# Kernel optimization log

Hardware: AMD Instinct MI355X
Metric: run time of the kernel (lower is better)

## Reference

```python
import jax, jax.numpy as jnp
import numpy as np

B, T, D, H = 4, 2048, 1024, 16
HD = D // H  # head_dim = 64

def setup_inputs() -> dict:
    key = jax.random.key(0)
    ks = jax.random.split(key, 5)
    s = 0.02
    return {
        "x": jax.random.normal(ks[0], (B, T, D), jnp.float32),
        "Wq": jax.random.normal(ks[1], (D, D), jnp.float32) * s,
        "Wk": jax.random.normal(ks[2], (D, D), jnp.float32) * s,
        "Wv": jax.random.normal(ks[3], (D, D), jnp.float32) * s,
        "Wo": jax.random.normal(ks[4], (D, D), jnp.float32) * s,
        "bo": jnp.zeros((D,), jnp.float32),
    }

def reference(x, Wq, Wk, Wv, Wo, bo):
    b, t, _ = x.shape
    # projections (no qkv bias), split into heads: [b, H, t, hd]
    def split_heads(y):
        return y.reshape(b, t, H, HD).transpose(0, 2, 1, 3)
    q = split_heads(x @ Wq)
    k = split_heads(x @ Wk)
    v = split_heads(x @ Wv)
    # causal attention scores, scaled by sqrt(head_dim)
    scores = jnp.einsum('bhqd,bhkd->bhqk', q, k) / jnp.sqrt(jnp.float32(HD))
    causal = jnp.tril(jnp.ones((t, t), bool))  # True = keep
    scores = jnp.where(causal, scores, -jnp.inf)
    w = jax.nn.softmax(scores, axis=-1)
    # dropout p=0.0 -> identity (eval-mode math)
    z = jnp.einsum('bhqk,bhkd->bhqd', w, v)
    z = z.transpose(0, 2, 1, 3).reshape(b, t, D)
    return z @ Wo + bo
```

## Files before the change

### kernel.cpp

```cpp
#include <hip/hip_runtime.h>
#include <hip/hip_bf16.h>

#define B_ 4
#define T_ 2048
#define D_ 1024
#define H_ 16
#define HD_ 64
#define M_ (B_*T_)

#define QSCALE (0.125f * 1.44269504088896f)

typedef __bf16  bf16x8 __attribute__((ext_vector_type(8)));
typedef __bf16  bf16x4 __attribute__((ext_vector_type(4)));
typedef float   f32x4  __attribute__((ext_vector_type(4)));
typedef ushort  u16x8  __attribute__((ext_vector_type(8)));

__device__ __forceinline__ ushort f2bf(float f) {
  union { float f; uint u; } c; c.f = f;
  uint u = c.u;
  uint r = (u + 0x7FFFu + ((u >> 16) & 1u)) >> 16;
  return (ushort)r;
}

__device__ __forceinline__ void gload_lds16(const void* g, void* l) {
  __builtin_amdgcn_global_load_lds(
      (const __attribute__((address_space(1))) void*)g,
      (__attribute__((address_space(3))) void*)l, 16, 0, 0);
}

__global__ __launch_bounds__(256) void cast_bf16(const float* __restrict__ x,
                                                 ushort* __restrict__ o, int n) {
  int i = (blockIdx.x * 256 + threadIdx.x) * 8;
  if (i >= n) return;
  float4 a = *(const float4*)&x[i];
  float4 b = *(const float4*)&x[i + 4];
  u16x8 r;
  r[0] = f2bf(a.x); r[1] = f2bf(a.y); r[2] = f2bf(a.z); r[3] = f2bf(a.w);
  r[4] = f2bf(b.x); r[5] = f2bf(b.y); r[6] = f2bf(b.z); r[7] = f2bf(b.w);
  *(u16x8*)&o[i] = r;
}

__global__ __launch_bounds__(256) void transw(const float* __restrict__ W0,
                                              const float* __restrict__ W1,
                                              const float* __restrict__ W2,
                                              const float* __restrict__ W3,
                                              ushort* __restrict__ Wt) {
  __shared__ float tile[32][33];
  const float* W = (blockIdx.z == 0) ? W0 : (blockIdx.z == 1) ? W1
                  : (blockIdx.z == 2) ? W2 : W3;
  ushort* dst = Wt + (size_t)blockIdx.z * D_ * D_;
  int tx = threadIdx.x & 31, ty = threadIdx.x >> 5;
  int bx = blockIdx.x, by = blockIdx.y;
  #pragma unroll
  for (int i = 0; i < 4; ++i)
    tile[ty + i * 8][tx] = W[(by * 32 + ty + i * 8) * D_ + bx * 32 + tx];
  __syncthreads();
  #pragma unroll
  for (int i = 0; i < 4; ++i)
    dst[(bx * 32 + ty + i * 8) * D_ + by * 32 + tx] = f2bf(tile[tx][ty + i * 8]);
}

template<int EPI>
__global__ __launch_bounds__(256, 2) void gemm_bt(const ushort* __restrict__ A,
                                                  const ushort* __restrict__ Bt,
                                                  const float* __restrict__ bias,
                                                  ushort* __restrict__ Qb,
                                                  ushort* __restrict__ Kb,
                                                  ushort* __restrict__ Vt,
                                                  float* __restrict__ Out) {
  constexpr int MI  = (EPI == 0) ? 8 : 4;
  constexpr int BM  = MI * 32;
  constexpr int MSP = MI * 16;
  __shared__ __align__(16) ushort As[BM * 64];
  __shared__ __align__(16) ushort Bs[128 * 64];
  const int tid = threadIdx.x;
  const int l   = tid & 63;
  const int wid = tid >> 6;
  const int lr  = l & 15, lg = l >> 4;
  const int wm  = wid >> 1, wn = wid & 1;

  const int nwgx = gridDim.x;
  int bid = blockIdx.y * nwgx + blockIdx.x;
  int cpx = (nwgx * gridDim.y) >> 3;
  int swz = (bid & 7) * cpx + (bid >> 3);
  const int m0 = (swz / nwgx) * BM;
  const int n0 = (swz % nwgx) * 128;

  const int srow = l >> 3;
  const int sce  = ((l & 7) ^ srow) * 8;
  const int xr   = (lr & 7) << 4;
  const int ce0  = ((0  + lg * 16) ^ xr) >> 1;
  const int ce1  = ((64 + lg * 16) ^ xr) >> 1;

  f32x4 acc[MI][4];
  #pragma unroll
  for (int mi = 0; mi < MI; ++mi)
    #pragma unroll
    for (int ni = 0; ni < 4; ++ni)
      acc[mi][ni] = (f32x4){0.f, 0.f, 0.f, 0.f};

  #pragma unroll 1
  for (int k0 = 0; k0 < 1024; k0 += 64) {
    #pragma unroll
    for (int j = 0; j < MI; ++j) {
      int c = wid * MI + j;
      gload_lds16(&A[(size_t)(m0 + c * 8 + srow) * 1024 + k0 + sce],
                  &As[c * 512]);
    }
    #pragma unroll
    for (int j = 0; j < 4; ++j) {
      int c = wid * 4 + j;
      gload_lds16(&Bt[(size_t)(n0 + c * 8 + srow) * 1024 + k0 + sce],
                  &Bs[c * 512]);
    }
    __syncthreads();
    #pragma unroll
    for (int kk = 0; kk < 2; ++kk) {
      const int ce = kk ? ce1 : ce0;
      bf16x8 af[MI], bfv[4];
      #pragma unroll
      for (int mi = 0; mi < MI; ++mi)
        af[mi] = *(const bf16x8*)&As[(wm * MSP + mi * 16 + lr) * 64 + ce];
      #pragma unroll
      for (int ni = 0; ni < 4; ++ni)
        bfv[ni] = *(const bf16x8*)&Bs[(wn * 64 + ni * 16 + lr) * 64 + ce];
      __builtin_amdgcn_s_setprio(1);
      #pragma unroll
      for (int mi = 0; mi < MI; ++mi)
        #pragma unroll
        for (int ni = 0; ni < 4; ++ni)
          acc[mi][ni] = __builtin_amdgcn_mfma_f32_16x16x32_bf16(
              af[mi], bfv[ni], acc[mi][ni], 0, 0, 0);
      __builtin_amdgcn_s_setprio(0);
    }
    __syncthreads();
  }

  if (EPI == 0) {
    const int g = n0 >> 10;
    const int h = ((n0 & 1023) >> 6) + wn;
    if (g == 2) {
      #pragma unroll
      for (int mi = 0; mi < MI; ++mi) {
        int rr0 = m0 + wm * MSP + mi * 16 + lg * 4;
        int b = rr0 >> 11, t = rr0 & 2047;
        #pragma unroll
        for (int ni = 0; ni < 4; ++ni) {
          int hd = ni * 16 + lr;
          bf16x4 p4;
          #pragma unroll
          for (int r = 0; r < 4; ++r) p4[r] = (__bf16)acc[mi][ni][r];
          *(bf16x4*)&Vt[((size_t)(b * H_ + h) * HD_ + hd) * T_ + t] = p4;
        }
      }
    } else {
      #pragma unroll
      for (int mi = 0; mi < MI; ++mi)
        #pragma unroll
        for (int r = 0; r < 4; ++r) {
          int rr = m0 + wm * MSP + mi * 16 + lg * 4 + r;
          int b = rr >> 11, t = rr & 2047;
          #pragma unroll
          for (int ni = 0; ni < 4; ++ni) {
            int hd = ni * 16 + lr;
            float v = acc[mi][ni][r];
            if (g == 0) Qb[((size_t)(b * H_ + h) * T_ + t) * HD_ + hd] = f2bf(v * QSCALE);
            else        Kb[((size_t)(b * H_ + h) * T_ + t) * HD_ + hd] = f2bf(v);
          }
        }
    }
  } else {
    #pragma unroll
    for (int mi = 0; mi < MI; ++mi)
      #pragma unroll
      for (int ni = 0; ni < 4; ++ni) {
        int col = n0 + wn * 64 + ni * 16 + lr;
        float bv = bias[col];
        #pragma unroll
        for (int r = 0; r < 4; ++r) {
          int rr = m0 + wm * MSP + mi * 16 + lg * 4 + r;
          Out[(size_t)rr * 1024 + col] = acc[mi][ni][r] + bv;
        }
      }
  }
}

__global__ __launch_bounds__(256, 3) void attn_fwd(const ushort* __restrict__ Qb,
                                                   const ushort* __restrict__ Kb,
                                                   const ushort* __restrict__ Vt,
                                                   ushort* __restrict__ Z) {
  __shared__ __align__(16) ushort Ks[2][64 * 64];
  __shared__ __align__(16) ushort Vs[2][64 * 64];
  __shared__ __align__(16) ushort Plds[4][32 * 72];
  const int tid = threadIdx.x;
  const int l   = tid & 63;
  const int wid = tid >> 6;
  const int lr  = l & 15, lg = l >> 4;
  const int s   = blockIdx.x;
  const int idx = s >> 3;
  const int bh  = (s & 7) + 8 * (idx & 7);
  const int j   = 15 - (idx >> 3);
  const int q0  = j * 128;
  const int qw  = q0 + wid * 32;
  const int NT  = 2 * j + 2;
  const int myDiag = 2 * j + (wid >> 1);
  const ushort* Qh = Qb + (size_t)bh * T_ * HD_;
  const ushort* Kh = Kb + (size_t)bh * T_ * HD_;
  const ushort* Vh = Vt + (size_t)bh * HD_ * T_;
  ushort* Pl = &Plds[wid][0];

  const int srow = l >> 3;
  const int sce  = ((l & 7) ^ srow) * 8;
  const int xrE  = (lr & 7) * 8;
  const int ceK0 = (lg * 8) ^ xrE;
  const int ceK1 = (32 + lg * 8) ^ xrE;

  const int foff = lr * 64 + lg * 8;
  bf16x8 bq[2][2];
  #pragma unroll
  for (int qi = 0; qi < 2; ++qi)
    #pragma unroll
    for (int kk = 0; kk < 2; ++kk)
      bq[qi][kk] = *(const bf16x8*)&Qh[(qw + qi * 16) * 64 + kk * 32 + foff];

  f32x4 o[2][4];
  float l_[2] = {0.f, 0.f};
  #pragma unroll
  for (int mi = 0; mi < 2; ++mi)
    #pragma unroll
    for (int hi = 0; hi < 4; ++hi)
      o[mi][hi] = (f32x4){0.f, 0.f, 0.f, 0.f};

#define STAGEKV(BUF, KT)                                                        \
  {                                                                             \
    _Pragma("unroll")                                                           \
    for (int c = 0; c < 2; ++c) {                                               \
      int i = wid * 2 + c;                                                      \
      gload_lds16(&Kh[(size_t)((KT) * 64 + i * 8 + srow) * 64 + sce],           \
                  &Ks[BUF][i * 512]);                                           \
      gload_lds16(&Vh[(size_t)(i * 8 + srow) * T_ + (KT) * 64 + sce],           \
                  &Vs[BUF][i * 512]);                                           \
    }                                                                           \
  }

  STAGEKV(0, 0);
  __syncthreads();

  #pragma unroll 1
  for (int kt = 0; kt < NT; ++kt) {
    const int cur = kt & 1;
    if (kt + 1 < NT) STAGEKV(cur ^ 1, kt + 1);

    if (kt <= myDiag) {
      bf16x8 bk[4][2];
      #pragma unroll
      for (int ki = 0; ki < 4; ++ki) {
        bk[ki][0] = *(const bf16x8*)&Ks[cur][(ki * 16 + lr) * 64 + ceK0];
        bk[ki][1] = *(const bf16x8*)&Ks[cur][(ki * 16 + lr) * 64 + ceK1];
      }
      f32x4 st[4][2];
      #pragma unroll
      for (int ki = 0; ki < 4; ++ki)
        #pragma unroll
        for (int qi = 0; qi < 2; ++qi)
          st[ki][qi] = (f32x4){0.f, 0.f, 0.f, 0.f};
      __builtin_amdgcn_s_setprio(1);
      #pragma unroll
      for (int kk = 0; kk < 2; ++kk)
        #pragma unroll
        for (int ki = 0; ki < 4; ++ki)
          #pragma unroll
          for (int qi = 0; qi < 2; ++qi)
            st[ki][qi] = __builtin_amdgcn_mfma_f32_16x16x32_bf16(
                bk[ki][kk], bq[qi][kk], st[ki][qi], 0, 0, 0);
      __builtin_amdgcn_s_setprio(0);

      if (kt == myDiag) {
        const int qbase = qw - kt * 64;
        #pragma unroll
        for (int qi = 0; qi < 2; ++qi) {
          int qoff = qbase + qi * 16 + lr;
          #pragma unroll
          for (int ki = 0; ki < 4; ++ki)
            #pragma unroll
            for (int r = 0; r < 4; ++r)
              if (ki * 16 + lg * 4 + r > qoff) st[ki][qi][r] = -1e30f;
        }
      }

      #pragma unroll
      for (int qi = 0; qi < 2; ++qi) {
        float rs = 0.f;
        #pragma unroll
        for (int ki = 0; ki < 4; ++ki) {
          bf16x4 p4;
          #pragma unroll
          for (int r = 0; r < 4; ++r) {
            float p = exp2f(st[ki][qi][r]);
            rs += p;
            p4[r] = (__bf16)p;
          }
          *(bf16x4*)&Pl[(qi * 16 + lr) * 72 + ki * 16 + lg * 4] = p4;
        }
        l_[qi] += rs;
      }

      bf16x8 bv[4][2];
      #pragma unroll
      for (int hi = 0; hi < 4; ++hi) {
        bv[hi][0] = *(const bf16x8*)&Vs[cur][(hi * 16 + lr) * 64 + ceK0];
        bv[hi][1] = *(const bf16x8*)&Vs[cur][(hi * 16 + lr) * 64 + ceK1];
      }
      bf16x8 ap[2][2];
      #pragma unroll
      for (int mi = 0; mi < 2; ++mi)
        #pragma unroll
        for (int kk = 0; kk < 2; ++kk)
          ap[mi][kk] = *(const bf16x8*)&Pl[(mi * 16 + lr) * 72 + kk * 32 + lg * 8];
      __builtin_amdgcn_s_setprio(1);
      #pragma unroll
      for (int kk = 0; kk < 2; ++kk)
        #pragma unroll
        for (int mi = 0; mi < 2; ++mi)
          #pragma unroll
          for (int hi = 0; hi < 4; ++hi)
            o[mi][hi] = __builtin_amdgcn_mfma_f32_16x16x32_bf16(
                ap[mi][kk], bv[hi][kk], o[mi][hi], 0, 0, 0);
      __builtin_amdgcn_s_setprio(0);
    }
    __syncthreads();
  }
#undef STAGEKV

  #pragma unroll
  for (int mi = 0; mi < 2; ++mi) {
    l_[mi] += __shfl_xor(l_[mi], 16);
    l_[mi] += __shfl_xor(l_[mi], 32);
  }
  const int b = bh >> 4, h = bh & 15;
  #pragma unroll
  for (int mi = 0; mi < 2; ++mi)
    #pragma unroll
    for (int r = 0; r < 4; ++r) {
      float lv = __shfl(l_[mi], lg * 4 + r);
      float rinv = 1.f / lv;
      int t = qw + mi * 16 + lg * 4 + r;
      #pragma unroll
      for (int hi = 0; hi < 4; ++hi)
        Z[((size_t)(b * T_ + t)) * D_ + h * 64 + hi * 16 + lr] =
            f2bf(o[mi][hi][r] * rinv);
    }
}

extern "C" void kernel_launch(void* const* d_in, const int* in_sizes, int n_in,
                              void* d_out, int out_size, void* d_ws, size_t ws_size,
                              hipStream_t stream) {
  const float* x  = (const float*)d_in[0];
  const float* Wq = (const float*)d_in[1];
  const float* Wk = (const float*)d_in[2];
  const float* Wv = (const float*)d_in[3];
  const float* Wo = (const float*)d_in[4];
  const float* bo = (const float*)d_in[5];
  float* out = (float*)d_out;

  char* ws = (char*)d_ws;
  ushort* xb = (ushort*)(ws);
  ushort* Wt = (ushort*)(ws + 16777216);
  ushort* Qb = (ushort*)(ws + 25165824);
  ushort* Kb = (ushort*)(ws + 41943040);
  ushort* Vt = (ushort*)(ws + 58720256);
  ushort* Zb = (ushort*)(ws + 75497472);

  cast_bf16<<<4096, 256, 0, stream>>>(x, xb, M_ * D_);
  transw<<<dim3(32, 32, 4), 256, 0, stream>>>(Wq, Wk, Wv, Wo, Wt);
  gemm_bt<0><<<dim3(24, 32), 256, 0, stream>>>(xb, Wt, nullptr, Qb, Kb, Vt, nullptr);
  attn_fwd<<<1024, 256, 0, stream>>>(Qb, Kb, Vt, Zb);
  gemm_bt<1><<<dim3(8, 64), 256, 0, stream>>>(Zb, Wt + 3 * 1024 * 1024, bo,
                                              nullptr, nullptr, nullptr, out);
}
```

Baseline: 164.2 us.

## Swap MFMA operands for vectorized GEMM epilogues and compute softmax row sums via MFMA

In the projection GEMM, Q/K and output-projection tiles now swap MFMA A/B operands, so each lane holds four consecutive columns. This lets the epilogue write bf16x4 and float4 stores instead of scattered scalar stores. In attention, the row sum of P is computed by an extra MFMA against a ones vector rather than by scalar adds and cross-lane shuffles, and it is already laid out per row for normalization. The cost is extra MFMA work per tile and an operand-order branch in the GEMM inner loop.

```diff
diff --git a/kernel.cpp b/kernel.cpp
--- a/kernel.cpp
+++ b/kernel.cpp
@@ -86,6 +86,9 @@
   const int m0 = (swz / nwgx) * BM;
   const int n0 = (swz % nwgx) * 128;
 
+  const int g = (EPI == 0) ? (n0 >> 10) : -1;
+  const bool swp = (EPI == 1) || (g != 2);
+
   const int srow = l >> 3;
   const int sce  = ((l & 7) ^ srow) * 8;
   const int xr   = (lr & 7) << 4;
@@ -125,20 +128,28 @@
       for (int ni = 0; ni < 4; ++ni)
         bfv[ni] = *(const bf16x8*)&Bs[(wn * 64 + ni * 16 + lr) * 64 + ce];
       __builtin_amdgcn_s_setprio(1);
-      #pragma unroll
-      for (int mi = 0; mi < MI; ++mi)
-        #pragma unroll
-        for (int ni = 0; ni < 4; ++ni)
-          acc[mi][ni] = __builtin_amdgcn_mfma_f32_16x16x32_bf16(
-              af[mi], bfv[ni], acc[mi][ni], 0, 0, 0);
+      if (swp) {
+        #pragma unroll
+        for (int mi = 0; mi < MI; ++mi)
+          #pragma unroll
+          for (int ni = 0; ni < 4; ++ni)
+            acc[mi][ni] = __builtin_amdgcn_mfma_f32_16x16x32_bf16(
+                bfv[ni], af[mi], acc[mi][ni], 0, 0, 0);
+      } else {
+        #pragma unroll
+        for (int mi = 0; mi < MI; ++mi)
+          #pragma unroll
+          for (int ni = 0; ni < 4; ++ni)
+            acc[mi][ni] = __builtin_amdgcn_mfma_f32_16x16x32_bf16(
+                af[mi], bfv[ni], acc[mi][ni], 0, 0, 0);
+      }
       __builtin_amdgcn_s_setprio(0);
     }
     __syncthreads();
   }
 
   if (EPI == 0) {
-    const int g = n0 >> 10;
-    const int h = ((n0 & 1023) >> 6) + wn;
+    const int hb = ((n0 & 1023) >> 6) + wn;
     if (g == 2) {
       #pragma unroll
       for (int mi = 0; mi < MI; ++mi) {
@@ -150,38 +161,42 @@
           bf16x4 p4;
           #pragma unroll
           for (int r = 0; r < 4; ++r) p4[r] = (__bf16)acc[mi][ni][r];
-          *(bf16x4*)&Vt[((size_t)(b * H_ + h) * HD_ + hd) * T_ + t] = p4;
+          *(bf16x4*)&Vt[((size_t)(b * H_ + hb) * HD_ + hd) * T_ + t] = p4;
         }
       }
     } else {
-      #pragma unroll
-      for (int mi = 0; mi < MI; ++mi)
-        #pragma unroll
-        for (int r = 0; r < 4; ++r) {
-          int rr = m0 + wm * MSP + mi * 16 + lg * 4 + r;
-          int b = rr >> 11, t = rr & 2047;
-          #pragma unroll
-          for (int ni = 0; ni < 4; ++ni) {
-            int hd = ni * 16 + lr;
-            float v = acc[mi][ni][r];
-            if (g == 0) Qb[((size_t)(b * H_ + h) * T_ + t) * HD_ + hd] = f2bf(v * QSCALE);
-            else        Kb[((size_t)(b * H_ + h) * T_ + t) * HD_ + hd] = f2bf(v);
-          }
-        }
+      const float sc = (g == 0) ? QSCALE : 1.0f;
+      ushort* dst = (g == 0) ? Qb : Kb;
+      #pragma unroll
+      for (int mi = 0; mi < MI; ++mi) {
+        int rr = m0 + wm * MSP + mi * 16 + lr;
+        int b = rr >> 11, t = rr & 2047;
+        #pragma unroll
+        for (int ni = 0; ni < 4; ++ni) {
+          int hd0 = ni * 16 + lg * 4;
+          bf16x4 p4;
+          #pragma unroll
+          for (int r = 0; r < 4; ++r) p4[r] = (__bf16)(acc[mi][ni][r] * sc);
+          *(bf16x4*)&dst[((size_t)(b * H_ + hb) * T_ + t) * HD_ + hd0] = p4;
+        }
+      }
     }
   } else {
     #pragma unroll
-    for (int mi = 0; mi < MI; ++mi)
+    for (int mi = 0; mi < MI; ++mi) {
+      int rr = m0 + wm * MSP + mi * 16 + lr;
       #pragma unroll
       for (int ni = 0; ni < 4; ++ni) {
-        int col = n0 + wn * 64 + ni * 16 + lr;
-        float bv = bias[col];
-        #pragma unroll
-        for (int r = 0; r < 4; ++r) {
-          int rr = m0 + wm * MSP + mi * 16 + lg * 4 + r;
-          Out[(size_t)rr * 1024 + col] = acc[mi][ni][r] + bv;
-        }
-      }
+        int cb = n0 + wn * 64 + ni * 16 + lg * 4;
+        float4 bv = *(const float4*)&bias[cb];
+        float4 f4;
+        f4.x = acc[mi][ni][0] + bv.x;
+        f4.y = acc[mi][ni][1] + bv.y;
+        f4.z = acc[mi][ni][2] + bv.z;
+        f4.w = acc[mi][ni][3] + bv.w;
+        *(float4*)&Out[(size_t)rr * 1024 + cb] = f4;
+      }
+    }
   }
 }
 
@@ -223,13 +238,19 @@
     for (int kk = 0; kk < 2; ++kk)
       bq[qi][kk] = *(const bf16x8*)&Qh[(qw + qi * 16) * 64 + kk * 32 + foff];
 
+  bf16x8 vones;
+  #pragma unroll
+  for (int jj = 0; jj < 8; ++jj) vones[jj] = (__bf16)1.0f;
+
   f32x4 o[2][4];
-  float l_[2] = {0.f, 0.f};
-  #pragma unroll
-  for (int mi = 0; mi < 2; ++mi)
+  f32x4 accL[2];
+  #pragma unroll
+  for (int mi = 0; mi < 2; ++mi) {
+    accL[mi] = (f32x4){0.f, 0.f, 0.f, 0.f};
     #pragma unroll
     for (int hi = 0; hi < 4; ++hi)
       o[mi][hi] = (f32x4){0.f, 0.f, 0.f, 0.f};
+  }
 
 #define STAGEKV(BUF, KT)                                                        \
   {                                                                             \
@@ -289,21 +310,14 @@
       }
 
       #pragma unroll
-      for (int qi = 0; qi < 2; ++qi) {
-        float rs = 0.f;
+      for (int qi = 0; qi < 2; ++qi)
         #pragma unroll
         for (int ki = 0; ki < 4; ++ki) {
           bf16x4 p4;
           #pragma unroll
-          for (int r = 0; r < 4; ++r) {
-            float p = exp2f(st[ki][qi][r]);
-            rs += p;
-            p4[r] = (__bf16)p;
-          }
+          for (int r = 0; r < 4; ++r) p4[r] = (__bf16)exp2f(st[ki][qi][r]);
           *(bf16x4*)&Pl[(qi * 16 + lr) * 72 + ki * 16 + lg * 4] = p4;
         }
-        l_[qi] += rs;
-      }
 
       bf16x8 bv[4][2];
       #pragma unroll
@@ -321,29 +335,26 @@
       #pragma unroll
       for (int kk = 0; kk < 2; ++kk)
         #pragma unroll
-        for (int mi = 0; mi < 2; ++mi)
+        for (int mi = 0; mi < 2; ++mi) {
           #pragma unroll
           for (int hi = 0; hi < 4; ++hi)
             o[mi][hi] = __builtin_amdgcn_mfma_f32_16x16x32_bf16(
                 ap[mi][kk], bv[hi][kk], o[mi][hi], 0, 0, 0);
+          accL[mi] = __builtin_amdgcn_mfma_f32_16x16x32_bf16(
+              ap[mi][kk], vones, accL[mi], 0, 0, 0);
+        }
       __builtin_amdgcn_s_setprio(0);
     }
     __syncthreads();
   }
 #undef STAGEKV
 
-  #pragma unroll
-  for (int mi = 0; mi < 2; ++mi) {
-    l_[mi] += __shfl_xor(l_[mi], 16);
-    l_[mi] += __shfl_xor(l_[mi], 32);
-  }
   const int b = bh >> 4, h = bh & 15;
   #pragma unroll
   for (int mi = 0; mi < 2; ++mi)
     #pragma unroll
     for (int r = 0; r < 4; ++r) {
-      float lv = __shfl(l_[mi], lg * 4 + r);
-      float rinv = 1.f / lv;
+      float rinv = 1.f / accL[mi][r];
       int t = qw + mi * 16 + lg * 4 + r;
       #pragma unroll
       for (int hi = 0; hi < 4; ++hi)
```

Measured after the change: 546.3 us. 233% more time.
